# Optimization experiments

Measured on AMD Instinct MI355X. Metric: run time of the kernel, lower is better.

The kernel has to match this reference:

```python
import jax, jax.numpy as jnp
import numpy as np

BATCH, DIM, L, N = 2, 768, 2048, 16


def setup_inputs() -> dict:
    key = jax.random.key(0)
    ks = jax.random.split(key, 8)
    u = jax.random.normal(ks[0], (BATCH, DIM, L), dtype=jnp.float32)
    delta = jax.random.uniform(ks[1], (BATCH, DIM, L), dtype=jnp.float32)
    # A must be negative for a stable SSM (exp(delta*A) <= 1)
    A = -jax.random.uniform(ks[2], (DIM, N), dtype=jnp.float32, minval=0.5, maxval=1.5)
    B = jax.random.normal(ks[3], (BATCH, N, L), dtype=jnp.float32)
    C = jax.random.normal(ks[4], (BATCH, N, L), dtype=jnp.float32)
    D = jax.random.normal(ks[5], (DIM,), dtype=jnp.float32)
    z = jax.random.normal(ks[6], (BATCH, DIM, L), dtype=jnp.float32)
    delta_bias = 0.1 * jax.random.normal(ks[7], (DIM,), dtype=jnp.float32)
    return {"u": u, "delta": delta, "A": A, "B": B, "C": C,
            "D": D, "z": z, "delta_bias": delta_bias}


def _selective_scan(u, delta, A, B, C, D, z, delta_bias):
    # delta_softplus=True path of mamba_ssm selective_scan_fn
    delta = jax.nn.softplus(delta + delta_bias[None, :, None])  # (b, d, l)
    # discretize: deltaA = exp(delta * A), deltaB_u = delta * B * u
    deltaA = jnp.exp(jnp.einsum('bdl,dn->lbdn', delta, A))          # (l, b, d, n)
    deltaBu = jnp.einsum('bdl,bnl,bdl->lbdn', delta, B, u)          # (l, b, d, n)
    C_t = jnp.transpose(C, (2, 0, 1))                               # (l, b, n)

    def step(x, inp):
        a, bu, c = inp
        x = a * x + bu                                              # (b, d, n)
        y = jnp.einsum('bdn,bn->bd', x, c)                          # (b, d)
        return x, y

    x0 = jnp.zeros((BATCH, DIM, N), dtype=u.dtype)
    _, ys = jax.lax.scan(step, x0, (deltaA, deltaBu, C_t))          # ys: (l, b, d)
    y = jnp.transpose(ys, (1, 2, 0))                                # (b, d, l)
    out = y + u * D[None, :, None]
    out = out * jax.nn.silu(z)
    return out


def reference(u, delta, A, B, C, D, z, delta_bias):
    return _selective_scan(u, delta, A, B, C, D, z, delta_bias)
```

## Files before the change

kernel.cpp:

```cpp
#include <hip/hip_runtime.h>


#define LOG2E 1.4426950408889634f
#define LN2   0.6931471805599453f

constexpr int BATCH = 2, DIM = 768, L = 2048, N = 16;
constexpr int NC = 128, LC = 16;
constexpr int DG = DIM / 64;
constexpr int CPB = 4;
constexpr int CG = NC / CPB;
constexpr int NBLK = BATCH * DG * CG;
constexpr int NCOMB = BATCH * DIM * N;
constexpr int PAD = 76;
static_assert(NC * LC == L, "chunking must cover L");

__device__ __forceinline__ float fexp2(float x) { return __builtin_amdgcn_exp2f(x); }
__device__ __forceinline__ float softplus(float v) {
  float s = LN2 * __log2f(1.0f + fexp2(v * LOG2E));
  return (v > 20.0f) ? v : s;
}
__device__ __forceinline__ float silu(float v) { return v / (1.0f + fexp2(-v * LOG2E)); }

__global__ __launch_bounds__(256, 6) void k_pass1(
    const float* __restrict__ u, const float* __restrict__ delta,
    const float* __restrict__ A, const float* __restrict__ dbias,
    const float* __restrict__ Bg, float* __restrict__ h, float* __restrict__ S)
{
  __shared__ float ds_[64][PAD];
  __shared__ float Bsr[64][20];

  const int bid = blockIdx.x, t = threadIdx.x;
  const int cgi = bid & 31;
  const int dgb = bid >> 5;
  const int dg = dgb % DG;
  const int b = dgb / DG;
  const int d0 = dg * 64, l0 = cgi * 64;

  const int w = t >> 6, lane = t & 63;
  const int c = cgi * CPB + w;
  const int d = d0 + lane;
  const int row16 = t >> 4;
  const int col4 = (t & 15) * 4;

  const long ubase = ((long)(b * DIM + d)) * L + c * LC;
  float4 u0 = *(const float4*)(u + ubase + 0);
  float4 u1 = *(const float4*)(u + ubase + 4);
  float4 u2 = *(const float4*)(u + ubase + 8);
  float4 u3 = *(const float4*)(u + ubase + 12);

  float4 dreg[4];
#pragma unroll
  for (int rr = 0; rr < 4; rr++) {
    int row = row16 + rr * 16;
    long gof = ((long)(b * DIM + d0 + row)) * L + l0 + col4;
    dreg[rr] = *(const float4*)(delta + gof);
  }
  long bof = ((long)(b * N + row16)) * L + l0 + col4;
  float4 breg = *(const float4*)(Bg + bof);

  float A2[N];
#pragma unroll
  for (int q = 0; q < 4; q++) {
    float4 av = *(const float4*)(A + d * N + q * 4);
    A2[q*4+0] = av.x * LOG2E; A2[q*4+1] = av.y * LOG2E;
    A2[q*4+2] = av.z * LOG2E; A2[q*4+3] = av.w * LOG2E;
  }
  const float bias = dbias[d];

#pragma unroll
  for (int rr = 0; rr < 4; rr++) {
    int row = row16 + rr * 16;
    *(float4*)&ds_[row][col4] = dreg[rr];
  }
  Bsr[col4 + 0][row16] = breg.x;
  Bsr[col4 + 1][row16] = breg.y;
  Bsr[col4 + 2][row16] = breg.z;
  Bsr[col4 + 3][row16] = breg.w;

  float uu[LC];
  uu[0]=u0.x; uu[1]=u0.y; uu[2]=u0.z; uu[3]=u0.w;
  uu[4]=u1.x; uu[5]=u1.y; uu[6]=u1.z; uu[7]=u1.w;
  uu[8]=u2.x; uu[9]=u2.y; uu[10]=u2.z; uu[11]=u2.w;
  uu[12]=u3.x; uu[13]=u3.y; uu[14]=u3.z; uu[15]=u3.w;

  __syncthreads();

  float sp[LC], Ssum = 0.f;
#pragma unroll
  for (int q = 0; q < 4; q++) {
    float4 dv = *(const float4*)&ds_[lane][w * LC + q * 4];
    sp[q*4+0] = softplus(dv.x + bias);
    sp[q*4+1] = softplus(dv.y + bias);
    sp[q*4+2] = softplus(dv.z + bias);
    sp[q*4+3] = softplus(dv.w + bias);
  }
#pragma unroll
  for (int j = 0; j < LC; j++) Ssum += sp[j];

  float x[N];
#pragma unroll
  for (int n = 0; n < N; n++) x[n] = 0.f;
#pragma unroll
  for (int j = 0; j < LC; j++) {
    const int row = w * LC + j;
    float bb[16];
#pragma unroll
    for (int q = 0; q < 4; q++) {
      float4 bv = *(const float4*)&Bsr[row][q * 4];
      bb[q*4+0] = bv.x; bb[q*4+1] = bv.y; bb[q*4+2] = bv.z; bb[q*4+3] = bv.w;
    }
    float du = sp[j] * uu[j];
#pragma unroll
    for (int n = 0; n < N; n++) {
      float a = fexp2(sp[j] * A2[n]);
      x[n] = a * x[n] + du * bb[n];
    }
  }

  const long hb = (((long)(b * NC + c)) * DIM + d) * N;
#pragma unroll
  for (int q = 0; q < 4; q++) {
    float4 v; v.x = x[q*4+0]; v.y = x[q*4+1]; v.z = x[q*4+2]; v.w = x[q*4+3];
    *(float4*)(h + hb + q * 4) = v;
  }
  S[(b * NC + c) * DIM + d] = Ssum;
}

__global__ __launch_bounds__(128) void k_pass2(
    const float* __restrict__ h, const float* __restrict__ S,
    const float* __restrict__ A, float* __restrict__ hI)
{
  int g = blockIdx.x * 128 + threadIdx.x;
  int n = g & 15;
  int r = g >> 4;
  int dd = r % DIM;
  int bb = r / DIM;
  const float a2 = A[dd * N + n] * LOG2E;
  const long step = (long)DIM * N;
  const long base0 = (((long)bb * NC) * DIM + dd) * N + n;
  const long sbase = (long)(bb * NC) * DIM + dd;

  float x = 0.f;
  for (int cb = 0; cb < NC / 16; cb++) {
    float hc[16], Sc[16];
#pragma unroll
    for (int k = 0; k < 16; k++) {
      hc[k] = h[base0 + (long)(cb * 16 + k) * step];
      Sc[k] = S[sbase + (long)(cb * 16 + k) * DIM];
    }
#pragma unroll
    for (int k = 0; k < 16; k++) {
      hI[base0 + (long)(cb * 16 + k) * step] = x;
      x = fexp2(Sc[k] * a2) * x + hc[k];
    }
  }
}

__global__ __launch_bounds__(256, 4) void k_pass3(
    const float* __restrict__ u, const float* __restrict__ delta,
    const float* __restrict__ A, const float* __restrict__ dbias,
    const float* __restrict__ Bg, const float* __restrict__ Cg,
    const float* __restrict__ Dv, const float* __restrict__ z,
    const float* __restrict__ xinit, float* __restrict__ out)
{
  __shared__ float ds_[64][PAD];
  __shared__ float Bsr[64][20];
  __shared__ float Csr[64][20];

  const int bid = blockIdx.x, t = threadIdx.x;
  const int cgi = bid & 31;
  const int dgb = bid >> 5;
  const int dg = dgb % DG;
  const int b = dgb / DG;
  const int d0 = dg * 64, l0 = cgi * 64;

  const int w = t >> 6, lane = t & 63;
  const int c = cgi * CPB + w;
  const int d = d0 + lane;
  const int row16 = t >> 4;
  const int col4 = (t & 15) * 4;

  const long ubase = ((long)(b * DIM + d)) * L + c * LC;
  float4 u0 = *(const float4*)(u + ubase + 0);
  float4 u1 = *(const float4*)(u + ubase + 4);
  float4 u2 = *(const float4*)(u + ubase + 8);
  float4 u3 = *(const float4*)(u + ubase + 12);

  float4 dreg[4], zreg[4];
#pragma unroll
  for (int rr = 0; rr < 4; rr++) {
    int row = row16 + rr * 16;
    long gof = ((long)(b * DIM + d0 + row)) * L + l0 + col4;
    dreg[rr] = *(const float4*)(delta + gof);
    zreg[rr] = *(const float4*)(z + gof);
  }
  long bof = ((long)(b * N + row16)) * L + l0 + col4;
  float4 breg = *(const float4*)(Bg + bof);
  float4 creg = *(const float4*)(Cg + bof);

  const long hb = (((long)(b * NC + c)) * DIM + d) * N;
  float x[N];
#pragma unroll
  for (int q = 0; q < 4; q++) {
    float4 v = *(const float4*)(xinit + hb + q * 4);
    x[q*4+0] = v.x; x[q*4+1] = v.y; x[q*4+2] = v.z; x[q*4+3] = v.w;
  }

  float A2[N];
#pragma unroll
  for (int q = 0; q < 4; q++) {
    float4 av = *(const float4*)(A + d * N + q * 4);
    A2[q*4+0] = av.x * LOG2E; A2[q*4+1] = av.y * LOG2E;
    A2[q*4+2] = av.z * LOG2E; A2[q*4+3] = av.w * LOG2E;
  }
  const float bias = dbias[d];

#pragma unroll
  for (int rr = 0; rr < 4; rr++) {
    int row = row16 + rr * 16;
    *(float4*)&ds_[row][col4] = dreg[rr];
  }
  Bsr[col4 + 0][row16] = breg.x;
  Bsr[col4 + 1][row16] = breg.y;
  Bsr[col4 + 2][row16] = breg.z;
  Bsr[col4 + 3][row16] = breg.w;
  Csr[col4 + 0][row16] = creg.x;
  Csr[col4 + 1][row16] = creg.y;
  Csr[col4 + 2][row16] = creg.z;
  Csr[col4 + 3][row16] = creg.w;

  float uu[LC];
  uu[0]=u0.x; uu[1]=u0.y; uu[2]=u0.z; uu[3]=u0.w;
  uu[4]=u1.x; uu[5]=u1.y; uu[6]=u1.z; uu[7]=u1.w;
  uu[8]=u2.x; uu[9]=u2.y; uu[10]=u2.z; uu[11]=u2.w;
  uu[12]=u3.x; uu[13]=u3.y; uu[14]=u3.z; uu[15]=u3.w;

  __syncthreads();

  float sp[LC];
#pragma unroll
  for (int q = 0; q < 4; q++) {
    float4 dv = *(const float4*)&ds_[lane][w * LC + q * 4];
    sp[q*4+0] = softplus(dv.x + bias);
    sp[q*4+1] = softplus(dv.y + bias);
    sp[q*4+2] = softplus(dv.z + bias);
    sp[q*4+3] = softplus(dv.w + bias);
  }

  float y[LC];
#pragma unroll
  for (int j = 0; j < LC; j++) {
    const int row = w * LC + j;
    float bb[16], ccv[16];
#pragma unroll
    for (int q = 0; q < 4; q++) {
      float4 bv = *(const float4*)&Bsr[row][q * 4];
      float4 cv = *(const float4*)&Csr[row][q * 4];
      bb[q*4+0] = bv.x; bb[q*4+1] = bv.y; bb[q*4+2] = bv.z; bb[q*4+3] = bv.w;
      ccv[q*4+0] = cv.x; ccv[q*4+1] = cv.y; ccv[q*4+2] = cv.z; ccv[q*4+3] = cv.w;
    }
    float du = sp[j] * uu[j];
    float acc = 0.f;
#pragma unroll
    for (int n = 0; n < N; n++) {
      float a = fexp2(sp[j] * A2[n]);
      x[n] = a * x[n] + du * bb[n];
      acc += x[n] * ccv[n];
    }
    y[j] = acc;
  }

  __syncthreads();
#pragma unroll
  for (int q = 0; q < 4; q++) {
    float4 v; v.x = y[q*4+0]; v.y = y[q*4+1]; v.z = y[q*4+2]; v.w = y[q*4+3];
    *(float4*)&ds_[lane][w * LC + q * 4] = v;
  }

  __syncthreads();

#pragma unroll
  for (int rr = 0; rr < 4; rr++) {
    int row = row16 + rr * 16;
    long gof = ((long)(b * DIM + d0 + row)) * L + l0 + col4;
    float4 zv = zreg[rr];
    float4 uv = *(const float4*)(u + gof);
    float4 yv = *(const float4*)&ds_[row][col4];
    float Dd2 = Dv[d0 + row];
    float4 ov;
    ov.x = (yv.x + uv.x * Dd2) * silu(zv.x);
    ov.y = (yv.y + uv.y * Dd2) * silu(zv.y);
    ov.z = (yv.z + uv.z * Dd2) * silu(zv.z);
    ov.w = (yv.w + uv.w * Dd2) * silu(zv.w);
    *(float4*)(out + gof) = ov;
  }
}

__global__ __launch_bounds__(256) void k_simple(
    const float* __restrict__ u, const float* __restrict__ delta,
    const float* __restrict__ A, const float* __restrict__ dbias,
    const float* __restrict__ Bm, const float* __restrict__ Cm,
    const float* __restrict__ Dv, const float* __restrict__ z,
    float* __restrict__ out) {
  int t = blockIdx.x * 256 + threadIdx.x;
  int n = t % N;
  int bd = t / N;
  int d = bd % DIM;
  int b = bd / DIM;
  float A2 = A[d * N + n] * LOG2E;
  float bias = dbias[d];
  float Dd = Dv[d];
  const float* Bp = Bm + ((long)b * N + n) * L;
  const float* Cp = Cm + ((long)b * N + n) * L;
  long base = (long)bd * L;
  float x = 0.0f;
  for (int l = 0; l < L; l++) {
    float dv = delta[base + l];
    float uv = u[base + l];
    float sp = softplus(dv + bias);
    float a = fexp2(sp * A2);
    x = a * x + sp * uv * Bp[l];
    float y = x * Cp[l];
#pragma unroll
    for (int off = 8; off; off >>= 1) y += __shfl_xor(y, off, 16);
    if (n == 0) {
      float zv = z[base + l];
      out[base + l] = (y + uv * Dd) * silu(zv);
    }
  }
}

extern "C" void kernel_launch(void* const* d_in, const int* in_sizes, int n_in,
                              void* d_out, int out_size, void* d_ws, size_t ws_size,
                              hipStream_t stream) {
  const float* u     = (const float*)d_in[0];
  const float* delta = (const float*)d_in[1];
  const float* A     = (const float*)d_in[2];
  const float* Bm    = (const float*)d_in[3];
  const float* Cm    = (const float*)d_in[4];
  const float* Dv    = (const float*)d_in[5];
  const float* z     = (const float*)d_in[6];
  const float* dbias = (const float*)d_in[7];
  float* out = (float*)d_out;

  const size_t hp  = (size_t)BATCH * NC * DIM * N;
  const size_t spn = (size_t)BATCH * NC * DIM;
  const size_t need = (2 * hp + spn) * sizeof(float);

  if (ws_size < need) {
    k_simple<<<(BATCH * DIM * N) / 256, 256, 0, stream>>>(u, delta, A, dbias, Bm, Cm, Dv, z, out);
    return;
  }

  float* h  = (float*)d_ws;
  float* S  = h + hp;
  float* hI = S + spn;

  k_pass1<<<NBLK, 256, 0, stream>>>(u, delta, A, dbias, Bm, h, S);
  k_pass2<<<NCOMB / 128, 128, 0, stream>>>(h, S, A, hI);
  k_pass3<<<NBLK, 256, 0, stream>>>(u, delta, A, dbias, Bm, Cm, Dv, z, hI, out);
}
```

Before: 129.7 us.

## Store chunk states and softplus(delta) in bf16, reuse softplus in pass3

Pass 1 now writes the softplus(delta) values and the chunk-end states as packed bf16, and pass 2 reads and writes the states in bf16. Pass 3 reads the cached softplus values instead of reloading delta and recomputing softplus. This is meant to cut global memory traffic between the three kernels and remove transcendental work in pass 3. In exchange, the intermediate states and timesteps lose precision, and pass 2 now does narrow 2-byte strided accesses.

```diff
diff --git a/kernel.cpp b/kernel.cpp
--- a/kernel.cpp
+++ b/kernel.cpp
@@ -21,10 +21,20 @@
 }
 __device__ __forceinline__ float silu(float v) { return v / (1.0f + fexp2(-v * LOG2E)); }
 
+__device__ __forceinline__ unsigned pack2bf(float a, float b) {
+  unsigned ua = __float_as_uint(a), ub = __float_as_uint(b);
+  unsigned ra = (ua + 0x7FFFu + ((ua >> 16) & 1u)) >> 16;
+  unsigned rb = (ub + 0x7FFFu + ((ub >> 16) & 1u)) >> 16;
+  return ra | (rb << 16);
+}
+__device__ __forceinline__ float lo_bf(unsigned p) { return __uint_as_float(p << 16); }
+__device__ __forceinline__ float hi_bf(unsigned p) { return __uint_as_float(p & 0xFFFF0000u); }
+
 __global__ __launch_bounds__(256, 6) void k_pass1(
     const float* __restrict__ u, const float* __restrict__ delta,
     const float* __restrict__ A, const float* __restrict__ dbias,
-    const float* __restrict__ Bg, float* __restrict__ h, float* __restrict__ S)
+    const float* __restrict__ Bg, unsigned* __restrict__ h,
+    unsigned* __restrict__ spg, float* __restrict__ S)
 {
   __shared__ float ds_[64][PAD];
   __shared__ float Bsr[64][20];
@@ -97,6 +107,17 @@
 #pragma unroll
   for (int j = 0; j < LC; j++) Ssum += sp[j];
 
+  const long sb8 = (((long)(b * NC + c)) * DIM + d) * 8;
+  {
+    uint4 w0, w1;
+    w0.x = pack2bf(sp[0], sp[1]);  w0.y = pack2bf(sp[2], sp[3]);
+    w0.z = pack2bf(sp[4], sp[5]);  w0.w = pack2bf(sp[6], sp[7]);
+    w1.x = pack2bf(sp[8], sp[9]);  w1.y = pack2bf(sp[10], sp[11]);
+    w1.z = pack2bf(sp[12], sp[13]); w1.w = pack2bf(sp[14], sp[15]);
+    *(uint4*)(spg + sb8) = w0;
+    *(uint4*)(spg + sb8 + 4) = w1;
+  }
+
   float x[N];
 #pragma unroll
   for (int n = 0; n < N; n++) x[n] = 0.f;
@@ -117,18 +138,21 @@
     }
   }
 
-  const long hb = (((long)(b * NC + c)) * DIM + d) * N;
-#pragma unroll
-  for (int q = 0; q < 4; q++) {
-    float4 v; v.x = x[q*4+0]; v.y = x[q*4+1]; v.z = x[q*4+2]; v.w = x[q*4+3];
-    *(float4*)(h + hb + q * 4) = v;
+  {
+    uint4 w0, w1;
+    w0.x = pack2bf(x[0], x[1]);   w0.y = pack2bf(x[2], x[3]);
+    w0.z = pack2bf(x[4], x[5]);   w0.w = pack2bf(x[6], x[7]);
+    w1.x = pack2bf(x[8], x[9]);   w1.y = pack2bf(x[10], x[11]);
+    w1.z = pack2bf(x[12], x[13]); w1.w = pack2bf(x[14], x[15]);
+    *(uint4*)(h + sb8) = w0;
+    *(uint4*)(h + sb8 + 4) = w1;
   }
   S[(b * NC + c) * DIM + d] = Ssum;
 }
 
 __global__ __launch_bounds__(128) void k_pass2(
-    const float* __restrict__ h, const float* __restrict__ S,
-    const float* __restrict__ A, float* __restrict__ hI)
+    const unsigned* __restrict__ h, const float* __restrict__ S,
+    const float* __restrict__ A, unsigned* __restrict__ hI)
 {
   int g = blockIdx.x * 128 + threadIdx.x;
   int n = g & 15;
@@ -136,8 +160,10 @@
   int dd = r % DIM;
   int bb = r / DIM;
   const float a2 = A[dd * N + n] * LOG2E;
-  const long step = (long)DIM * N;
-  const long base0 = (((long)bb * NC) * DIM + dd) * N + n;
+  const unsigned short* hs = (const unsigned short*)h;
+  unsigned short* hIs = (unsigned short*)hI;
+  const long step = (long)DIM * 16;
+  const long base0 = (((long)bb * NC) * DIM + dd) * 16 + n;
   const long sbase = (long)(bb * NC) * DIM + dd;
 
   float x = 0.f;
@@ -145,25 +171,28 @@
     float hc[16], Sc[16];
 #pragma unroll
     for (int k = 0; k < 16; k++) {
-      hc[k] = h[base0 + (long)(cb * 16 + k) * step];
+      unsigned short hv = hs[base0 + (long)(cb * 16 + k) * step];
+      hc[k] = __uint_as_float(((unsigned)hv) << 16);
       Sc[k] = S[sbase + (long)(cb * 16 + k) * DIM];
     }
 #pragma unroll
     for (int k = 0; k < 16; k++) {
-      hI[base0 + (long)(cb * 16 + k) * step] = x;
+      unsigned ux = __float_as_uint(x);
+      hIs[base0 + (long)(cb * 16 + k) * step] =
+          (unsigned short)((ux + 0x7FFFu + ((ux >> 16) & 1u)) >> 16);
       x = fexp2(Sc[k] * a2) * x + hc[k];
     }
   }
 }
 
 __global__ __launch_bounds__(256, 4) void k_pass3(
-    const float* __restrict__ u, const float* __restrict__ delta,
-    const float* __restrict__ A, const float* __restrict__ dbias,
+    const float* __restrict__ u, const float* __restrict__ A,
     const float* __restrict__ Bg, const float* __restrict__ Cg,
     const float* __restrict__ Dv, const float* __restrict__ z,
-    const float* __restrict__ xinit, float* __restrict__ out)
+    const unsigned* __restrict__ xinit, const unsigned* __restrict__ spg,
+    float* __restrict__ out)
 {
-  __shared__ float ds_[64][PAD];
+  __shared__ float ys[64][PAD];
   __shared__ float Bsr[64][20];
   __shared__ float Csr[64][20];
 
@@ -186,25 +215,22 @@
   float4 u2 = *(const float4*)(u + ubase + 8);
   float4 u3 = *(const float4*)(u + ubase + 12);
 
-  float4 dreg[4], zreg[4];
+  const long sb8 = (((long)(b * NC + c)) * DIM + d) * 8;
+  uint4 sp0 = *(const uint4*)(spg + sb8);
+  uint4 sp1 = *(const uint4*)(spg + sb8 + 4);
+  uint4 xi0 = *(const uint4*)(xinit + sb8);
+  uint4 xi1 = *(const uint4*)(xinit + sb8 + 4);
+
+  float4 zreg[4];
 #pragma unroll
   for (int rr = 0; rr < 4; rr++) {
     int row = row16 + rr * 16;
     long gof = ((long)(b * DIM + d0 + row)) * L + l0 + col4;
-    dreg[rr] = *(const float4*)(delta + gof);
     zreg[rr] = *(const float4*)(z + gof);
   }
   long bof = ((long)(b * N + row16)) * L + l0 + col4;
   float4 breg = *(const float4*)(Bg + bof);
   float4 creg = *(const float4*)(Cg + bof);
-
-  const long hb = (((long)(b * NC + c)) * DIM + d) * N;
-  float x[N];
-#pragma unroll
-  for (int q = 0; q < 4; q++) {
-    float4 v = *(const float4*)(xinit + hb + q * 4);
-    x[q*4+0] = v.x; x[q*4+1] = v.y; x[q*4+2] = v.z; x[q*4+3] = v.w;
-  }
 
   float A2[N];
 #pragma unroll
@@ -213,13 +239,7 @@
     A2[q*4+0] = av.x * LOG2E; A2[q*4+1] = av.y * LOG2E;
     A2[q*4+2] = av.z * LOG2E; A2[q*4+3] = av.w * LOG2E;
   }
-  const float bias = dbias[d];
-
-#pragma unroll
-  for (int rr = 0; rr < 4; rr++) {
-    int row = row16 + rr * 16;
-    *(float4*)&ds_[row][col4] = dreg[rr];
-  }
+
   Bsr[col4 + 0][row16] = breg.x;
   Bsr[col4 + 1][row16] = breg.y;
   Bsr[col4 + 2][row16] = breg.z;
@@ -235,17 +255,19 @@
   uu[8]=u2.x; uu[9]=u2.y; uu[10]=u2.z; uu[11]=u2.w;
   uu[12]=u3.x; uu[13]=u3.y; uu[14]=u3.z; uu[15]=u3.w;
 
+  float sp[LC];
+  sp[0]=lo_bf(sp0.x); sp[1]=hi_bf(sp0.x); sp[2]=lo_bf(sp0.y); sp[3]=hi_bf(sp0.y);
+  sp[4]=lo_bf(sp0.z); sp[5]=hi_bf(sp0.z); sp[6]=lo_bf(sp0.w); sp[7]=hi_bf(sp0.w);
+  sp[8]=lo_bf(sp1.x); sp[9]=hi_bf(sp1.x); sp[10]=lo_bf(sp1.y); sp[11]=hi_bf(sp1.y);
+  sp[12]=lo_bf(sp1.z); sp[13]=hi_bf(sp1.z); sp[14]=lo_bf(sp1.w); sp[15]=hi_bf(sp1.w);
+
+  float x[N];
+  x[0]=lo_bf(xi0.x); x[1]=hi_bf(xi0.x); x[2]=lo_bf(xi0.y); x[3]=hi_bf(xi0.y);
+  x[4]=lo_bf(xi0.z); x[5]=hi_bf(xi0.z); x[6]=lo_bf(xi0.w); x[7]=hi_bf(xi0.w);
+  x[8]=lo_bf(xi1.x); x[9]=hi_bf(xi1.x); x[10]=lo_bf(xi1.y); x[11]=hi_bf(xi1.y);
+  x[12]=lo_bf(xi1.z); x[13]=hi_bf(xi1.z); x[14]=lo_bf(xi1.w); x[15]=hi_bf(xi1.w);
+
   __syncthreads();
-
-  float sp[LC];
-#pragma unroll
-  for (int q = 0; q < 4; q++) {
-    float4 dv = *(const float4*)&ds_[lane][w * LC + q * 4];
-    sp[q*4+0] = softplus(dv.x + bias);
-    sp[q*4+1] = softplus(dv.y + bias);
-    sp[q*4+2] = softplus(dv.z + bias);
-    sp[q*4+3] = softplus(dv.w + bias);
-  }
 
   float y[LC];
 #pragma unroll
@@ -270,11 +292,10 @@
     y[j] = acc;
   }
 
-  __syncthreads();
 #pragma unroll
   for (int q = 0; q < 4; q++) {
     float4 v; v.x = y[q*4+0]; v.y = y[q*4+1]; v.z = y[q*4+2]; v.w = y[q*4+3];
-    *(float4*)&ds_[lane][w * LC + q * 4] = v;
+    *(float4*)&ys[lane][w * LC + q * 4] = v;
   }
 
   __syncthreads();
@@ -285,7 +306,7 @@
     long gof = ((long)(b * DIM + d0 + row)) * L + l0 + col4;
     float4 zv = zreg[rr];
     float4 uv = *(const float4*)(u + gof);
-    float4 yv = *(const float4*)&ds_[row][col4];
+    float4 yv = *(const float4*)&ys[row][col4];
     float Dd2 = Dv[d0 + row];
     float4 ov;
     ov.x = (yv.x + uv.x * Dd2) * silu(zv.x);
@@ -343,20 +364,21 @@
   const float* dbias = (const float*)d_in[7];
   float* out = (float*)d_out;
 
-  const size_t hp  = (size_t)BATCH * NC * DIM * N;
+  const size_t hp8 = (size_t)BATCH * NC * DIM * 8;
   const size_t spn = (size_t)BATCH * NC * DIM;
-  const size_t need = (2 * hp + spn) * sizeof(float);
+  const size_t need = (3 * hp8 + spn) * sizeof(unsigned);
 
   if (ws_size < need) {
     k_simple<<<(BATCH * DIM * N) / 256, 256, 0, stream>>>(u, delta, A, dbias, Bm, Cm, Dv, z, out);
     return;
   }
 
-  float* h  = (float*)d_ws;
-  float* S  = h + hp;
-  float* hI = S + spn;
-
-  k_pass1<<<NBLK, 256, 0, stream>>>(u, delta, A, dbias, Bm, h, S);
+  unsigned* h   = (unsigned*)d_ws;
+  unsigned* hI  = h + hp8;
+  unsigned* spg = hI + hp8;
+  float* S      = (float*)(spg + hp8);
+
+  k_pass1<<<NBLK, 256, 0, stream>>>(u, delta, A, dbias, Bm, h, spg, S);
   k_pass2<<<NCOMB / 128, 128, 0, stream>>>(h, S, A, hI);
-  k_pass3<<<NBLK, 256, 0, stream>>>(u, delta, A, dbias, Bm, Cm, Dv, z, hI, out);
-}
+  k_pass3<<<NBLK, 256, 0, stream>>>(u, A, Bm, Cm, Dv, z, hI, spg, out);
+}
```

Measured after the change: 141.1 us. 1.09x slower.
